# Kernel optimization log

Hardware: AMD Instinct MI355X
Metric: run time of the kernel (lower is better)

## Reference

```python
import jax, jax.numpy as jnp
import numpy as np

EPS = 1e-12
LORA_RANK = 16

def setup_inputs() -> dict:
    key = jax.random.key(0)
    ks = jax.random.split(key, 7)
    bs, sq, din, dout = 8, 2048, 2048, 2048
    n_tasks, n_splits, n_skills, r = 32, 1, 8, LORA_RANK
    return {
        'x': jax.random.normal(ks[0], (bs, sq, din), dtype=jnp.float32),
        'W': jax.random.normal(ks[1], (dout, din), dtype=jnp.float32) * (1.0 / np.sqrt(din)),
        'b': jax.random.normal(ks[2], (dout,), dtype=jnp.float32) * 0.02,
        'module_logits': jax.random.normal(ks[3], (n_tasks, n_splits * n_skills), dtype=jnp.float32) * 0.001,
        'A': jax.random.normal(ks[4], (n_splits, n_skills, din // n_splits, r), dtype=jnp.float32) * 0.02,
        'B': jax.random.normal(ks[5], (n_splits, n_skills, r, dout // n_splits), dtype=jnp.float32) * 0.02,
        'tasks': jax.random.randint(ks[6], (bs,), 0, n_tasks),
    }

def reference(x, W, b, module_logits, A, B, tasks):
    bs, sq, din = x.shape
    n_splits, n_skills, _, r = A.shape
    dout = W.shape[0]
    # Polytropon selector (eval mode): sigmoid + normalize over skills
    probs = jax.nn.sigmoid(module_logits[tasks]).reshape(bs, n_splits, n_skills)
    probs = probs / (probs.sum(-1, keepdims=True) + EPS)  # [bs, p, t]
    # WeightedSum combinor: per-example skill mixture of LoRA params
    A_c = jnp.einsum('bpt,ptir->bpir', probs, A)  # [bs, p, din/p, r]
    B_c = jnp.einsum('bpt,ptro->bpro', probs, B)  # [bs, p, r, dout/p]
    # LoRA forward: reshape to per-example [din, r] and [r, dout]
    A_r = A_c.reshape(bs, din, r)
    B_r = jnp.transpose(B_c, (0, 2, 1, 3)).reshape(bs, r, dout)
    lora = jnp.einsum('bsr,bro->bso', jnp.einsum('bsi,bir->bsr', x, A_r), B_r)
    base = jnp.einsum('bsi,oi->bso', x, W) + b
    return base + lora * (1.0 / r)
```

## Files before the change

kernel.cpp:

```cpp
#include <hip/hip_runtime.h>

typedef __attribute__((ext_vector_type(4))) float f32x4;
typedef __attribute__((ext_vector_type(8))) short bf16x8;

__device__ __forceinline__ unsigned short f2b(float f) {
  unsigned u = __float_as_uint(f);
  u = (u + 0x7FFFu + ((u >> 16) & 1u)) >> 16;
  return (unsigned short)u;
}

__device__ __forceinline__ void gload_lds16(unsigned short* lds, const unsigned short* g) {
  __builtin_amdgcn_global_load_lds(
      (const __attribute__((address_space(1))) unsigned int*)(g),
      (__attribute__((address_space(3))) unsigned int*)(lds), 16, 0, 0);
}

__global__ void combine_kernel(const float* __restrict__ logits,
                               const int*   __restrict__ tasks,
                               const float* __restrict__ A,
                               const float* __restrict__ B,
                               unsigned short* __restrict__ Art,
                               unsigned short* __restrict__ Brt)
{
  int idx = blockIdx.x * 256 + threadIdx.x;
  int b = idx >> 11;
  int i = idx & 2047;
  if (b >= 8) return;
  int task = tasks[b];
  float p[8]; float s = 0.f;
  #pragma unroll
  for (int t = 0; t < 8; ++t) {
    float l = logits[task * 8 + t];
    float e = 1.f / (1.f + __expf(-l));
    p[t] = e; s += e;
  }
  float inv = 1.f / (s + 1e-12f);
  #pragma unroll
  for (int t = 0; t < 8; ++t) p[t] *= inv;

  float ar[16];
  #pragma unroll
  for (int r = 0; r < 16; ++r) ar[r] = 0.f;
  for (int t = 0; t < 8; ++t) {
    const float* ap = A + ((size_t)t * 2048 + i) * 16;
    float pt = p[t];
    #pragma unroll
    for (int r = 0; r < 16; ++r) ar[r] += pt * ap[r];
  }
  #pragma unroll
  for (int r = 0; r < 16; ++r)
    Art[((size_t)b * 16 + r) * 2048 + i] = f2b(ar[r]);

  float br[16];
  #pragma unroll
  for (int r = 0; r < 16; ++r) br[r] = 0.f;
  for (int t = 0; t < 8; ++t) {
    float pt = p[t];
    #pragma unroll
    for (int r = 0; r < 16; ++r) br[r] += pt * B[((size_t)t * 16 + r) * 2048 + i];
  }
  #pragma unroll
  for (int r = 0; r < 16; ++r)
    Brt[((size_t)b * 2048 + i) * 16 + r] = f2b(br[r] * 0.0625f);
}

__global__ void wconv_kernel(const float* __restrict__ W, unsigned short* __restrict__ Wb) {
  size_t i = ((size_t)blockIdx.x * 256 + threadIdx.x) * 4;
  f32x4 v = *(const f32x4*)(W + i);
  ushort4 o;
  o.x = f2b(v.x); o.y = f2b(v.y); o.z = f2b(v.z); o.w = f2b(v.w);
  *(ushort4*)(Wb + i) = o;
}

__global__ void xa_conv_kernel(const float* __restrict__ x,
                               const unsigned short* __restrict__ Art,
                               unsigned short* __restrict__ xb,
                               unsigned short* __restrict__ xa)
{
  __shared__ unsigned short As[64 * 64];
  int tid = threadIdx.x;
  int lane = tid & 63;
  int wv = tid >> 6;
  int rowbase = blockIdx.x * 64;
  int batch = rowbase >> 11;
  int lr = lane & 15, hi = lane >> 4;
  f32x4 acc; acc.x = 0.f; acc.y = 0.f; acc.z = 0.f; acc.w = 0.f;

  for (int k0 = 0; k0 < 2048; k0 += 64) {
    #pragma unroll
    for (int p = 0; p < 4; ++p) {
      int row = p * 16 + (tid >> 4);
      int k = (tid & 15) * 4;
      f32x4 v = *(const f32x4*)(x + (size_t)(rowbase + row) * 2048 + k0 + k);
      ushort4 o;
      o.x = f2b(v.x); o.y = f2b(v.y); o.z = f2b(v.z); o.w = f2b(v.w);
      *(ushort4*)(xb + (size_t)(rowbase + row) * 2048 + k0 + k) = o;
      *(ushort4*)(As + row * 64 + k) = o;
    }
    __syncthreads();
    #pragma unroll
    for (int kk = 0; kk < 64; kk += 32) {
      bf16x8 a = *(const bf16x8*)(As + (wv * 16 + lr) * 64 + kk + hi * 8);
      bf16x8 bf = *(const bf16x8*)(Art + ((size_t)batch * 16 + lr) * 2048 + k0 + kk + hi * 8);
      acc = __builtin_amdgcn_mfma_f32_16x16x32_bf16(a, bf, acc, 0, 0, 0);
    }
    __syncthreads();
  }
  #pragma unroll
  for (int j = 0; j < 4; ++j) {
    int row = rowbase + wv * 16 + hi * 4 + j;
    xa[(size_t)row * 16 + lr] = f2b(acc[j]);
  }
}

__global__ void gemm_kernel(const unsigned short* __restrict__ xb,
                            const unsigned short* __restrict__ Wb,
                            const float* __restrict__ bias,
                            const unsigned short* __restrict__ xa,
                            const unsigned short* __restrict__ Brt,
                            float* __restrict__ out)
{
  __shared__ unsigned short As[128 * 64];
  __shared__ unsigned short Bs[128 * 64];
  int tid = threadIdx.x;
  int lane = tid & 63;
  int wv = tid >> 6;
  int wr = wv >> 1, wc = wv & 1;
  int bid = blockIdx.x;
  int tn = bid & 15, tm = bid >> 4;
  int rowbase = tm * 128, colbase = tn * 128;
  int lr = lane & 15, hi = lane >> 4;

  f32x4 acc[4][4];
  #pragma unroll
  for (int m = 0; m < 4; ++m)
    #pragma unroll
    for (int n = 0; n < 4; ++n) { acc[m][n].x = 0.f; acc[m][n].y = 0.f; acc[m][n].z = 0.f; acc[m][n].w = 0.f; }

  for (int k0 = 0; k0 < 2048; k0 += 64) {
    #pragma unroll
    for (int i = 0; i < 4; ++i) {
      int c = tid + i * 256;
      int row = c >> 3, kc = c & 7;
      gload_lds16(As + c * 8, xb + (size_t)(rowbase + row) * 2048 + k0 + kc * 8);
    }
    #pragma unroll
    for (int i = 0; i < 4; ++i) {
      int c = tid + i * 256;
      int row = c >> 3, kc = c & 7;
      gload_lds16(Bs + c * 8, Wb + (size_t)(colbase + row) * 2048 + k0 + kc * 8);
    }
    __syncthreads();
    #pragma unroll
    for (int kk = 0; kk < 64; kk += 32) {
      bf16x8 a[4], bb[4];
      #pragma unroll
      for (int m = 0; m < 4; ++m)
        a[m] = *(const bf16x8*)(As + (wr * 64 + m * 16 + lr) * 64 + kk + hi * 8);
      #pragma unroll
      for (int n = 0; n < 4; ++n)
        bb[n] = *(const bf16x8*)(Bs + (wc * 64 + n * 16 + lr) * 64 + kk + hi * 8);
      #pragma unroll
      for (int m = 0; m < 4; ++m)
        #pragma unroll
        for (int n = 0; n < 4; ++n)
          acc[m][n] = __builtin_amdgcn_mfma_f32_16x16x32_bf16(a[m], bb[n], acc[m][n], 0, 0, 0);
    }
    __syncthreads();
  }

  int batch = rowbase >> 11;
  bf16x8 zf = (bf16x8)(short)0;
  bf16x8 av[4], bv[4];
  #pragma unroll
  for (int m = 0; m < 4; ++m) {
    if (hi < 2)
      av[m] = *(const bf16x8*)(xa + (size_t)(rowbase + wr * 64 + m * 16 + lr) * 16 + hi * 8);
    else
      av[m] = zf;
  }
  #pragma unroll
  for (int n = 0; n < 4; ++n) {
    if (hi < 2)
      bv[n] = *(const bf16x8*)(Brt + ((size_t)batch * 2048 + colbase + wc * 64 + n * 16 + lr) * 16 + hi * 8);
    else
      bv[n] = zf;
  }
  #pragma unroll
  for (int m = 0; m < 4; ++m)
    #pragma unroll
    for (int n = 0; n < 4; ++n)
      acc[m][n] = __builtin_amdgcn_mfma_f32_16x16x32_bf16(av[m], bv[n], acc[m][n], 0, 0, 0);

  #pragma unroll
  for (int n = 0; n < 4; ++n) {
    int col = colbase + wc * 64 + n * 16 + lr;
    float bbv = bias[col];
    #pragma unroll
    for (int m = 0; m < 4; ++m) {
      int row0 = rowbase + wr * 64 + m * 16 + hi * 4;
      #pragma unroll
      for (int j = 0; j < 4; ++j)
        out[(size_t)(row0 + j) * 2048 + col] = acc[m][n][j] + bbv;
    }
  }
}

extern "C" void kernel_launch(void* const* d_in, const int* in_sizes, int n_in,
                              void* d_out, int out_size, void* d_ws, size_t ws_size,
                              hipStream_t stream) {
  const float* x      = (const float*)d_in[0];
  const float* W      = (const float*)d_in[1];
  const float* bias   = (const float*)d_in[2];
  const float* logits = (const float*)d_in[3];
  const float* A      = (const float*)d_in[4];
  const float* B      = (const float*)d_in[5];
  const int*   tasks  = (const int*)d_in[6];
  float* out = (float*)d_out;

  char* ws = (char*)d_ws;
  unsigned short* xb  = (unsigned short*)(ws);
  unsigned short* Wb  = (unsigned short*)(ws + 67108864);
  unsigned short* xa  = (unsigned short*)(ws + 67108864 + 8388608);
  unsigned short* Art = (unsigned short*)(ws + 67108864 + 8388608 + 524288);
  unsigned short* Brt = (unsigned short*)(ws + 67108864 + 8388608 + 1048576);

  combine_kernel<<<64, 256, 0, stream>>>(logits, tasks, A, B, Art, Brt);
  wconv_kernel<<<4096, 256, 0, stream>>>(W, Wb);
  xa_conv_kernel<<<256, 256, 0, stream>>>(x, Art, xb, xa);
  gemm_kernel<<<2048, 256, 0, stream>>>(xb, Wb, bias, xa, Brt, out);
}
```

Baseline: 225.5 us.

## Rewrite GEMM with 256x256 tiles, double-buffered swizzled LDS and interleaved prefetch

Replaces the 128x128 bf16 GEMM with a 512-thread, 256x256-tile kernel. It uses 128KB of double-buffered LDS with XOR-swizzled rows and a grouped block-order swizzle. The k-loop is split into four quarter-stages, each interleaving global-to-LDS prefetch of the next tiles with MFMA work, using explicit vmcnt waits, raw barriers and setprio. The goal is more data reuse per loaded byte, fewer LDS bank conflicts and hidden load latency, at the cost of high register and LDS pressure and fragile hand-managed synchronisation.

```diff
diff --git a/kernel.cpp b/kernel.cpp
--- a/kernel.cpp
+++ b/kernel.cpp
@@ -9,11 +9,8 @@
   return (unsigned short)u;
 }
 
-__device__ __forceinline__ void gload_lds16(unsigned short* lds, const unsigned short* g) {
-  __builtin_amdgcn_global_load_lds(
-      (const __attribute__((address_space(1))) unsigned int*)(g),
-      (__attribute__((address_space(3))) unsigned int*)(lds), 16, 0, 0);
-}
+#define BAR() asm volatile("s_barrier" ::: "memory")
+#define VMCNT(N) asm volatile("s_waitcnt vmcnt(" #N ")" ::: "memory")
 
 __global__ void combine_kernel(const float* __restrict__ logits,
                                const int*   __restrict__ tasks,
@@ -113,71 +110,135 @@
   }
 }
 
-__global__ void gemm_kernel(const unsigned short* __restrict__ xb,
-                            const unsigned short* __restrict__ Wb,
-                            const float* __restrict__ bias,
-                            const unsigned short* __restrict__ xa,
-                            const unsigned short* __restrict__ Brt,
-                            float* __restrict__ out)
+__global__ __launch_bounds__(512, 2)
+void gemm_kernel(const unsigned short* __restrict__ xb,
+                 const unsigned short* __restrict__ Wb,
+                 const float* __restrict__ bias,
+                 const unsigned short* __restrict__ xa,
+                 const unsigned short* __restrict__ Brt,
+                 float* __restrict__ out)
 {
-  __shared__ unsigned short As[128 * 64];
-  __shared__ unsigned short Bs[128 * 64];
-  int tid = threadIdx.x;
-  int lane = tid & 63;
-  int wv = tid >> 6;
-  int wr = wv >> 1, wc = wv & 1;
-  int bid = blockIdx.x;
-  int tn = bid & 15, tm = bid >> 4;
-  int rowbase = tm * 128, colbase = tn * 128;
-  int lr = lane & 15, hi = lane >> 4;
-
-  f32x4 acc[4][4];
-  #pragma unroll
-  for (int m = 0; m < 4; ++m)
-    #pragma unroll
-    for (int n = 0; n < 4; ++n) { acc[m][n].x = 0.f; acc[m][n].y = 0.f; acc[m][n].z = 0.f; acc[m][n].w = 0.f; }
-
-  for (int k0 = 0; k0 < 2048; k0 += 64) {
-    #pragma unroll
-    for (int i = 0; i < 4; ++i) {
-      int c = tid + i * 256;
-      int row = c >> 3, kc = c & 7;
-      gload_lds16(As + c * 8, xb + (size_t)(rowbase + row) * 2048 + k0 + kc * 8);
-    }
-    #pragma unroll
-    for (int i = 0; i < 4; ++i) {
-      int c = tid + i * 256;
-      int row = c >> 3, kc = c & 7;
-      gload_lds16(Bs + c * 8, Wb + (size_t)(colbase + row) * 2048 + k0 + kc * 8);
-    }
-    __syncthreads();
-    #pragma unroll
-    for (int kk = 0; kk < 64; kk += 32) {
-      bf16x8 a[4], bb[4];
-      #pragma unroll
-      for (int m = 0; m < 4; ++m)
-        a[m] = *(const bf16x8*)(As + (wr * 64 + m * 16 + lr) * 64 + kk + hi * 8);
-      #pragma unroll
-      for (int n = 0; n < 4; ++n)
-        bb[n] = *(const bf16x8*)(Bs + (wc * 64 + n * 16 + lr) * 64 + kk + hi * 8);
-      #pragma unroll
-      for (int m = 0; m < 4; ++m)
-        #pragma unroll
-        for (int n = 0; n < 4; ++n)
-          acc[m][n] = __builtin_amdgcn_mfma_f32_16x16x32_bf16(a[m], bb[n], acc[m][n], 0, 0, 0);
-    }
-    __syncthreads();
-  }
-
-  int batch = rowbase >> 11;
+  __shared__ __align__(16) char lds[131072];
+  const int tid = threadIdx.x;
+  const int lane = tid & 63;
+  const int wv = tid >> 6;
+  const int wr = wv >> 2, wc = wv & 3;
+  const int lr = lane & 15, hi = lane >> 4;
+  const int hi16 = hi * 16;
+
+  const int bid = blockIdx.x;
+  const int swz = (bid & 7) * 64 + (bid >> 3);
+  const int tm = swz >> 3, tn = swz & 7;
+  const int rowbase = tm * 256, colbase = tn * 256;
+
+  const int row0 = tid >> 3;
+  const int cb0 = (tid & 7) * 16;
+  const int scb_e = (cb0 ^ ((row0 & 7) << 4)) >> 1;
+  const int rb5 = ((row0 >> 5) << 6) + (row0 & 31);
+
+#define GL16(LDSOFF, GPTR) \
+  __builtin_amdgcn_global_load_lds((const __attribute__((address_space(1))) unsigned int*)(GPTR), \
+      (__attribute__((address_space(3))) unsigned int*)(lds + (LDSOFF)), 16, 0, 0)
+
+#define STAGE_A(MH, DBUF, KOFF) { \
+  const unsigned short* g_ = xb + (size_t)(rowbase + (MH)*64 + row0) * 2048 + (KOFF) + scb_e; \
+  GL16((DBUF)*65536 + (MH)*16384 + tid*16, g_); \
+  GL16((DBUF)*65536 + (MH)*16384 + 8192 + tid*16, g_ + 128*2048); \
+}
+#define STAGE_B(NH, DBUF, KOFF) { \
+  const unsigned short* g_ = Wb + (size_t)(colbase + (NH)*32 + rb5) * 2048 + (KOFF) + scb_e; \
+  GL16((DBUF)*65536 + 32768 + (NH)*16384 + tid*16, g_); \
+  GL16((DBUF)*65536 + 32768 + (NH)*16384 + 8192 + tid*16, g_ + 128*2048); \
+}
+
+#define READ_A(MH) \
+  _Pragma("unroll") \
+  for (int mf = 0; mf < 4; ++mf) { \
+    int ar_ = (MH)*128 + wr*64 + mf*16 + lr; \
+    _Pragma("unroll") \
+    for (int kk = 0; kk < 2; ++kk) \
+      a[mf][kk] = *(const bf16x8*)(Ab + ar_*128 + ((kk*64 + hi16) ^ ((ar_&7)<<4))); \
+  }
+#define READ_B(NH, BREG) \
+  _Pragma("unroll") \
+  for (int nf = 0; nf < 2; ++nf) { \
+    int br_ = (NH)*128 + wc*32 + nf*16 + lr; \
+    _Pragma("unroll") \
+    for (int kk = 0; kk < 2; ++kk) \
+      BREG[nf][kk] = *(const bf16x8*)(Bb + br_*128 + ((kk*64 + hi16) ^ ((br_&7)<<4))); \
+  }
+#define MFMA_BLOCK(MH, NH, BREG) \
+  __builtin_amdgcn_s_setprio(1); \
+  _Pragma("unroll") \
+  for (int mf = 0; mf < 4; ++mf) \
+    _Pragma("unroll") \
+    for (int nf = 0; nf < 2; ++nf) \
+      _Pragma("unroll") \
+      for (int kk = 0; kk < 2; ++kk) \
+        acc[(MH)*4+mf][(NH)*2+nf] = __builtin_amdgcn_mfma_f32_16x16x32_bf16( \
+            a[mf][kk], BREG[nf][kk], acc[(MH)*4+mf][(NH)*2+nf], 0, 0, 0); \
+  __builtin_amdgcn_s_setprio(0);
+
+  f32x4 acc[8][4];
+  #pragma unroll
+  for (int i = 0; i < 8; ++i)
+    #pragma unroll
+    for (int n = 0; n < 4; ++n) { acc[i][n].x = 0.f; acc[i][n].y = 0.f; acc[i][n].z = 0.f; acc[i][n].w = 0.f; }
+
+  bf16x8 a[4][2], b0[2][2], b1[2][2];
+
+  STAGE_A(0, 0, 0);
+  STAGE_B(0, 0, 0);
+  STAGE_A(1, 0, 0);
+  STAGE_B(1, 0, 0);
+  STAGE_A(0, 1, 64);
+  STAGE_B(0, 1, 64);
+  VMCNT(4);
+  BAR();
+
+  for (int kt = 0; kt < 32; ++kt) {
+    const int buf = kt & 1, nbuf = buf ^ 1;
+    const char* Ab = lds + buf * 65536;
+    const char* Bb = Ab + 32768;
+    const int k1 = (kt + 1) * 64, k2 = (kt + 2) * 64;
+
+    READ_A(0);
+    READ_B(0, b0);
+    if (kt < 31) STAGE_A(1, nbuf, k1);
+    BAR();
+    MFMA_BLOCK(0, 0, b0);
+    if (kt < 31) { VMCNT(3); } else { VMCNT(0); }
+    BAR();
+
+    READ_B(1, b1);
+    if (kt < 31) STAGE_B(1, nbuf, k1);
+    BAR();
+    MFMA_BLOCK(0, 1, b1);
+    BAR();
+
+    READ_A(1);
+    if (kt < 30) STAGE_A(0, buf, k2);
+    BAR();
+    MFMA_BLOCK(1, 0, b0);
+    BAR();
+
+    if (kt < 30) STAGE_B(0, buf, k2);
+    BAR();
+    MFMA_BLOCK(1, 1, b1);
+    if (kt < 30) { VMCNT(4); }
+    else if (kt == 30) { VMCNT(2); }
+    BAR();
+  }
+
+  const int batch = rowbase >> 11;
   bf16x8 zf = (bf16x8)(short)0;
-  bf16x8 av[4], bv[4];
-  #pragma unroll
-  for (int m = 0; m < 4; ++m) {
+  bf16x8 av[8], bv[4];
+  #pragma unroll
+  for (int i = 0; i < 8; ++i) {
     if (hi < 2)
-      av[m] = *(const bf16x8*)(xa + (size_t)(rowbase + wr * 64 + m * 16 + lr) * 16 + hi * 8);
+      av[i] = *(const bf16x8*)(xa + (size_t)(rowbase + wr * 128 + i * 16 + lr) * 16 + hi * 8);
     else
-      av[m] = zf;
+      av[i] = zf;
   }
   #pragma unroll
   for (int n = 0; n < 4; ++n) {
@@ -187,23 +248,29 @@
       bv[n] = zf;
   }
   #pragma unroll
-  for (int m = 0; m < 4; ++m)
+  for (int i = 0; i < 8; ++i)
     #pragma unroll
     for (int n = 0; n < 4; ++n)
-      acc[m][n] = __builtin_amdgcn_mfma_f32_16x16x32_bf16(av[m], bv[n], acc[m][n], 0, 0, 0);
+      acc[i][n] = __builtin_amdgcn_mfma_f32_16x16x32_bf16(av[i], bv[n], acc[i][n], 0, 0, 0);
 
   #pragma unroll
   for (int n = 0; n < 4; ++n) {
     int col = colbase + wc * 64 + n * 16 + lr;
     float bbv = bias[col];
     #pragma unroll
-    for (int m = 0; m < 4; ++m) {
-      int row0 = rowbase + wr * 64 + m * 16 + hi * 4;
+    for (int i = 0; i < 8; ++i) {
+      int r0 = rowbase + wr * 128 + i * 16 + hi * 4;
       #pragma unroll
       for (int j = 0; j < 4; ++j)
-        out[(size_t)(row0 + j) * 2048 + col] = acc[m][n][j] + bbv;
+        out[(size_t)(r0 + j) * 2048 + col] = acc[i][n][j] + bbv;
     }
   }
+#undef GL16
+#undef STAGE_A
+#undef STAGE_B
+#undef READ_A
+#undef READ_B
+#undef MFMA_BLOCK
 }
 
 extern "C" void kernel_launch(void* const* d_in, const int* in_sizes, int n_in,
@@ -228,5 +295,5 @@
   combine_kernel<<<64, 256, 0, stream>>>(logits, tasks, A, B, Art, Brt);
   wconv_kernel<<<4096, 256, 0, stream>>>(W, Wb);
   xa_conv_kernel<<<256, 256, 0, stream>>>(x, Art, xb, xa);
-  gemm_kernel<<<2048, 256, 0, stream>>>(xb, Wb, bias, xa, Brt, out);
-}
+  gemm_kernel<<<512, 512, 0, stream>>>(xb, Wb, bias, xa, Brt, out);
+}
```

Result: faster. 206.5 us (-8.5%).
